# Kernel tuning notes

Hardware: AMD Instinct MI355X
Metric: run time of the kernel (lower is better)

Reference implementation:

```python
import jax, jax.numpy as jnp
import numpy as np

# Module constants derived from init kwargs:
# factor=3, indices_per_spike=64, index_maximum=19, border_pad=5
FACTOR = 3
IPS = 64            # indices_per_spike
INDEX_MAX = 19
BP = 5              # border_pad == width
CENTER = (INDEX_MAX + BP) * FACTOR          # 72
LO = CENTER - BP * FACTOR                   # 57
HI = CENTER + BP * FACTOR                   # 87
NEW_CENTER = LO                             # 57
ALIGNED_LEN = (IPS + 2 * BP) * FACTOR - 2 * BP * FACTOR  # 192


def setup_inputs() -> dict:
    key = jax.random.key(0)
    K, L = 500000, 220
    spikes_up = jax.random.normal(key, (K, L), dtype=jnp.float32)
    return {"spikes_up": spikes_up}


def reference(spikes_up):
    K, L = spikes_up.shape
    hi = min(HI, L)
    # per-row argmax in search window [LO, hi)
    window = spikes_up[:, LO:hi]                               # (K, hi-LO)
    local_peaks = jnp.argmax(window, axis=1)                   # (K,)
    index_max = local_peaks + LO
    starts = index_max - CENTER + BP * FACTOR                  # (K,)
    ends = starts + ALIGNED_LEN
    in_bounds = (starts >= 0) & (ends <= L)
    # shifted gather with clamped offsets
    safe_starts = jnp.clip(starts, 0, L - ALIGNED_LEN)
    offsets = jnp.arange(ALIGNED_LEN)
    all_indices = jnp.clip(safe_starts[:, None] + offsets[None, :], 0, L - 1)  # (K, 192)
    aligned = jnp.take_along_axis(spikes_up, all_indices, axis=1)              # (K, 192)
    # validity: peak must land exactly at NEW_CENTER and the slice in bounds
    at_center = jnp.argmax(aligned, axis=1) == NEW_CENTER
    valid = at_center & in_bounds
    removed_mask = ~valid
    # strided downsample (every FACTOR-th sample), invalid rows zeroed
    ds_idx = jnp.arange(IPS) * FACTOR
    downsampled = aligned[:, ds_idx]                           # (K, 64)
    spikes_final = jnp.where(valid[:, None], downsampled, jnp.zeros((), spikes_up.dtype))
    return spikes_final, removed_mask
```

## Files before the change

kernel.cpp:

```cpp
#include <hip/hip_runtime.h>
#include <cfloat>

#define LCOLS        220
#define WIN_LO       57
#define WIN_HI       86
#define ALIGNED_LEN_ 192
#define MAX_START    28
#define IPS_         64
#define NEW_CENTER_  57

__global__ __launch_bounds__(256, 4) void peak_align_kernel(
    const float* __restrict__ in,
    float* __restrict__ out_spikes,
    float* __restrict__ out_mask,
    int K)
{
    const int lane            = threadIdx.x & 63;
    const int wave_in_block   = threadIdx.x >> 6;
    const int waves_per_block = blockDim.x >> 6;
    const long long wave_id   = (long long)blockIdx.x * waves_per_block + wave_in_block;
    const long long nwaves    = (long long)gridDim.x * waves_per_block;

    for (long long r = wave_id; r < K; r += nwaves) {
        const float* row = in + r * (long long)LCOLS;
        const int c0 = lane * 4;

        float4 v = make_float4(-FLT_MAX, -FLT_MAX, -FLT_MAX, -FLT_MAX);
        if (lane < 55) v = *(const float4*)(row + c0);
        float e[4] = {v.x, v.y, v.z, v.w};

        float bv = -FLT_MAX; int bi = 0x7fffffff;
        #pragma unroll
        for (int k = 0; k < 4; ++k) {
            int c = c0 + k;
            if (c >= WIN_LO && c <= WIN_HI && e[k] > bv) { bv = e[k]; bi = c; }
        }
        #pragma unroll
        for (int off = 32; off >= 1; off >>= 1) {
            float ov = __shfl_xor(bv, off);
            int   oi = __shfl_xor(bi, off);
            if (ov > bv || (ov == bv && oi < bi)) { bv = ov; bi = oi; }
        }
        const int  index_max = bi;
        const int  start     = index_max - WIN_LO;
        const bool in_bounds = (start <= MAX_START);
        const int  s         = start > MAX_START ? MAX_START : start;

        float av = -FLT_MAX; int ai = 0x7fffffff;
        #pragma unroll
        for (int k = 0; k < 4; ++k) {
            int c = c0 + k;
            if (c >= s && c < s + ALIGNED_LEN_ && e[k] > av) { av = e[k]; ai = c; }
        }
        #pragma unroll
        for (int off = 32; off >= 1; off >>= 1) {
            float ov = __shfl_xor(av, off);
            int   oi = __shfl_xor(ai, off);
            if (ov > av || (ov == av && oi < ai)) { av = ov; ai = oi; }
        }
        const bool at_center = (ai == s + NEW_CENTER_);
        const bool valid     = at_center && in_bounds;

        int   c   = s + 3 * lane;
        int   src = c >> 2;
        int   sub = c & 3;
        float g0 = __shfl(e[0], src);
        float g1 = __shfl(e[1], src);
        float g2 = __shfl(e[2], src);
        float g3 = __shfl(e[3], src);
        float dv = (sub == 0) ? g0 : (sub == 1) ? g1 : (sub == 2) ? g2 : g3;

        out_spikes[r * IPS_ + lane] = valid ? dv : 0.0f;
        if (lane == 0) out_mask[r] = valid ? 0.0f : 1.0f;
    }
}

extern "C" void kernel_launch(void* const* d_in, const int* in_sizes, int n_in,
                              void* d_out, int out_size, void* d_ws, size_t ws_size,
                              hipStream_t stream) {
    const float* in = (const float*)d_in[0];
    const int K = in_sizes[0] / LCOLS;

    float* out_spikes = (float*)d_out;
    float* out_mask   = out_spikes + (long long)K * IPS_;

    const int block = 256;
    const int grid  = 4096;

    hipLaunchKernelGGL(peak_align_kernel, dim3(grid), dim3(block), 0, stream,
                       in, out_spikes, out_mask, K);
}
```

Baseline: 625.9 us.

## Stage 64-row tiles in LDS via async global_load_lds, one row per lane

```diff
diff --git a/kernel.cpp b/kernel.cpp
--- a/kernel.cpp
+++ b/kernel.cpp
@@ -8,71 +8,86 @@
 #define MAX_START    28
 #define IPS_         64
 #define NEW_CENTER_  57
+#define TILE_ROWS    64
+#define TILE_WORDS   (TILE_ROWS * LCOLS)
 
-__global__ __launch_bounds__(256, 4) void peak_align_kernel(
+__device__ __forceinline__ void async_copy16(const float* gsrc, float* ldst) {
+    __builtin_amdgcn_global_load_lds(
+        (const __attribute__((address_space(1))) void*)gsrc,
+        (__attribute__((address_space(3))) void*)ldst, 16, 0, 0);
+}
+
+__global__ __launch_bounds__(64) void peak_align_tile(
     const float* __restrict__ in,
     float* __restrict__ out_spikes,
     float* __restrict__ out_mask,
     int K)
 {
-    const int lane            = threadIdx.x & 63;
-    const int wave_in_block   = threadIdx.x >> 6;
-    const int waves_per_block = blockDim.x >> 6;
-    const long long wave_id   = (long long)blockIdx.x * waves_per_block + wave_in_block;
-    const long long nwaves    = (long long)gridDim.x * waves_per_block;
+    __shared__ __align__(16) float tile[TILE_WORDS];
+    __shared__ int srow[TILE_ROWS];
 
-    for (long long r = wave_id; r < K; r += nwaves) {
-        const float* row = in + r * (long long)LCOLS;
-        const int c0 = lane * 4;
+    const int lane = threadIdx.x;
+    const long long base = (long long)blockIdx.x * TILE_ROWS;
+    const int rows = (int)(((long long)K - base) < TILE_ROWS ? (K - base) : TILE_ROWS);
+    const float* src = in + base * LCOLS;
 
-        float4 v = make_float4(-FLT_MAX, -FLT_MAX, -FLT_MAX, -FLT_MAX);
-        if (lane < 55) v = *(const float4*)(row + c0);
-        float e[4] = {v.x, v.y, v.z, v.w};
+    const int bytes = rows * (LCOLS * 4);
+    const int nfull = bytes >> 10;
+    for (int it = 0; it < nfull; ++it) {
+        async_copy16(src + (it << 8) + lane * 4, &tile[it << 8]);
+    }
+    const int rem = bytes - (nfull << 10);
+    if (lane * 16 < rem) {
+        const float4 v = *(const float4*)(src + (nfull << 8) + lane * 4);
+        *(float4*)&tile[(nfull << 8) + lane * 4] = v;
+    }
+    __syncthreads();
 
-        float bv = -FLT_MAX; int bi = 0x7fffffff;
+    int  s_val = 0;
+    bool valid = false;
+    if (lane < rows) {
+        const float* row = &tile[lane * LCOLS];
+
+        float bv = -FLT_MAX; int bi = WIN_LO;
         #pragma unroll
-        for (int k = 0; k < 4; ++k) {
-            int c = c0 + k;
-            if (c >= WIN_LO && c <= WIN_HI && e[k] > bv) { bv = e[k]; bi = c; }
+        for (int j = 14; j <= 21; ++j) {
+            const float4 q = *(const float4*)(row + (j << 2));
+            const float qq[4] = {q.x, q.y, q.z, q.w};
+            #pragma unroll
+            for (int k = 0; k < 4; ++k) {
+                const int c = (j << 2) + k;
+                if (c >= WIN_LO && c <= WIN_HI && qq[k] > bv) { bv = qq[k]; bi = c; }
+            }
         }
-        #pragma unroll
-        for (int off = 32; off >= 1; off >>= 1) {
-            float ov = __shfl_xor(bv, off);
-            int   oi = __shfl_xor(bi, off);
-            if (ov > bv || (ov == bv && oi < bi)) { bv = ov; bi = oi; }
+        const int  start = bi - WIN_LO;
+        const bool in_b  = (start <= MAX_START);
+        const int  s     = in_b ? start : MAX_START;
+
+        float av = -FLT_MAX; int ai = -1;
+        #pragma unroll 5
+        for (int j = 0; j < 55; ++j) {
+            const float4 q = *(const float4*)(row + (j << 2));
+            const float qq[4] = {q.x, q.y, q.z, q.w};
+            #pragma unroll
+            for (int k = 0; k < 4; ++k) {
+                const int c = (j << 2) + k;
+                const bool inr = (unsigned)(c - s) < (unsigned)ALIGNED_LEN_;
+                if (inr && qq[k] > av) { av = qq[k]; ai = c; }
+            }
         }
-        const int  index_max = bi;
-        const int  start     = index_max - WIN_LO;
-        const bool in_bounds = (start <= MAX_START);
-        const int  s         = start > MAX_START ? MAX_START : start;
+        valid = in_b && (ai == s + NEW_CENTER_);
+        s_val = s;
+    }
+    srow[lane] = s_val | (valid ? (1 << 30) : 0);
+    __syncthreads();
 
-        float av = -FLT_MAX; int ai = 0x7fffffff;
-        #pragma unroll
-        for (int k = 0; k < 4; ++k) {
-            int c = c0 + k;
-            if (c >= s && c < s + ALIGNED_LEN_ && e[k] > av) { av = e[k]; ai = c; }
-        }
-        #pragma unroll
-        for (int off = 32; off >= 1; off >>= 1) {
-            float ov = __shfl_xor(av, off);
-            int   oi = __shfl_xor(ai, off);
-            if (ov > av || (ov == av && oi < ai)) { av = ov; ai = oi; }
-        }
-        const bool at_center = (ai == s + NEW_CENTER_);
-        const bool valid     = at_center && in_bounds;
-
-        int   c   = s + 3 * lane;
-        int   src = c >> 2;
-        int   sub = c & 3;
-        float g0 = __shfl(e[0], src);
-        float g1 = __shfl(e[1], src);
-        float g2 = __shfl(e[2], src);
-        float g3 = __shfl(e[3], src);
-        float dv = (sub == 0) ? g0 : (sub == 1) ? g1 : (sub == 2) ? g2 : g3;
-
-        out_spikes[r * IPS_ + lane] = valid ? dv : 0.0f;
-        if (lane == 0) out_mask[r] = valid ? 0.0f : 1.0f;
+    for (int rr = 0; rr < rows; ++rr) {
+        const int pk = srow[rr];
+        const int s  = pk & 0xFFFF;
+        const float v = tile[rr * LCOLS + s + 3 * lane];
+        out_spikes[(base + rr) * IPS_ + lane] = (pk & (1 << 30)) ? v : 0.0f;
     }
+    if (lane < rows) out_mask[base + lane] = valid ? 0.0f : 1.0f;
 }
 
 extern "C" void kernel_launch(void* const* d_in, const int* in_sizes, int n_in,
@@ -84,9 +99,7 @@
     float* out_spikes = (float*)d_out;
     float* out_mask   = out_spikes + (long long)K * IPS_;
 
-    const int block = 256;
-    const int grid  = 4096;
-
-    hipLaunchKernelGGL(peak_align_kernel, dim3(grid), dim3(block), 0, stream,
+    const int grid = (K + TILE_ROWS - 1) / TILE_ROWS;
+    hipLaunchKernelGGL(peak_align_tile, dim3(grid), dim3(TILE_ROWS), 0, stream,
                        in, out_spikes, out_mask, K);
 }
```

Result: no change. 636.9 us (+1.7%).
